# Performance work log

Measured on AMD Instinct MI355X. Metric: run time of the kernel, lower is better.

The kernel has to match this reference:

```python
import jax, jax.numpy as jnp
import numpy as np

EMBED_DIM = 1024
N_HEADS = 16
HEAD_SIZE = EMBED_DIM // N_HEADS
SEQ_LEN = 2048
BATCH = 4


def setup_inputs() -> dict:
    key = jax.random.key(0)
    ks = jax.random.split(key, 9)
    s = 0.02
    d = EMBED_DIM
    return {
        "x": jax.random.normal(ks[0], (BATCH, SEQ_LEN, d), dtype=jnp.float32),
        "wq": jax.random.normal(ks[1], (d, d), dtype=jnp.float32) * s,
        "bq": jnp.zeros((d,), dtype=jnp.float32),
        "wk": jax.random.normal(ks[2], (d, d), dtype=jnp.float32) * s,
        "bk": jnp.zeros((d,), dtype=jnp.float32),
        "wv": jax.random.normal(ks[3], (d, d), dtype=jnp.float32) * s,
        "bv": jnp.zeros((d,), dtype=jnp.float32),
        "wo": jax.random.normal(ks[4], (d, d), dtype=jnp.float32) * s,
        "bo": jnp.zeros((d,), dtype=jnp.float32),
    }


def reference(x, wq, bq, wk, bk, wv, bv, wo, bo):
    b, t, c = x.shape
    h, hs = N_HEADS, HEAD_SIZE
    scale = hs ** -0.5
    # projections (torch Linear: x @ W^T + b); here weights stored as [in, out]
    q = (x @ wq + bq).reshape(b, t, h, hs).transpose(0, 2, 1, 3)  # [b,h,t,hs]
    k = (x @ wk + bk).reshape(b, t, h, hs).transpose(0, 2, 1, 3)
    v = (x @ wv + bv).reshape(b, t, h, hs).transpose(0, 2, 1, 3)
    scores = jnp.einsum('bhqd,bhkd->bhqk', q, k) * scale  # [b,h,t,t]
    causal = jnp.tril(jnp.ones((t, t), dtype=bool))
    scores = jnp.where(causal, scores, -jnp.inf)
    probs = jax.nn.softmax(scores, axis=-1)
    attn = jnp.einsum('bhqk,bhkd->bhqd', probs, v)  # [b,h,t,hs]
    attn = attn.transpose(0, 2, 1, 3).reshape(b, t, c)
    return attn @ wo + bo
```

## Files before the change

kernel.cpp:

```cpp
#include <hip/hip_runtime.h>

#define EMBED 1024
#define NH 16
#define HS 64
#define SEQT 2048
#define NB 4

typedef unsigned short u16;
typedef unsigned int u32;
typedef __attribute__((ext_vector_type(8))) __bf16 bf16x8;
typedef __attribute__((ext_vector_type(4))) float f32x4;
typedef __attribute__((ext_vector_type(4))) unsigned short u16x4;

__device__ __forceinline__ u16 f2bf(float f) {
  __bf16 h = (__bf16)f;
  return __builtin_bit_cast(u16, h);
}

__device__ __forceinline__ void gload_lds16(const void* g, void* l) {
  __builtin_amdgcn_global_load_lds((const __attribute__((address_space(1))) void*)g,
                                   (__attribute__((address_space(3))) void*)l, 16, 0, 0);
}

#define MFMA16(a, b, c) __builtin_amdgcn_mfma_f32_16x16x32_bf16(a, b, c, 0, 0, 0)

__global__ void cvt_x(const float* __restrict__ in, u16* __restrict__ out) {
  int i = (blockIdx.x * 256 + threadIdx.x) * 4;
  float4 v = *(const float4*)(in + i);
  u16x4 o;
  o[0] = f2bf(v.x); o[1] = f2bf(v.y); o[2] = f2bf(v.z); o[3] = f2bf(v.w);
  *(u16x4*)(out + i) = o;
}

__global__ void wtrans(const float* __restrict__ w0, const float* __restrict__ w1,
                       const float* __restrict__ w2, const float* __restrict__ w3,
                       u16* __restrict__ t0, u16* __restrict__ t1,
                       u16* __restrict__ t2, u16* __restrict__ t3) {
  __shared__ float tile[32][33];
  const float* w; u16* t;
  switch (blockIdx.z) {
    case 0: w = w0; t = t0; break;
    case 1: w = w1; t = t1; break;
    case 2: w = w2; t = t2; break;
    default: w = w3; t = t3; break;
  }
  int n0 = blockIdx.x * 32, k0 = blockIdx.y * 32;
  int tx = threadIdx.x, ty = threadIdx.y;
#pragma unroll
  for (int r = 0; r < 4; ++r)
    tile[ty + r * 8][tx] = w[(size_t)(k0 + ty + r * 8) * EMBED + n0 + tx];
  __syncthreads();
#pragma unroll
  for (int r = 0; r < 4; ++r)
    t[(size_t)(n0 + ty + r * 8) * EMBED + k0 + tx] = f2bf(tile[tx][ty + r * 8]);
}

__global__ __launch_bounds__(256, 2) void gemm_qkv(
    const u16* __restrict__ A, const u16* __restrict__ Bt,
    const float* __restrict__ bq, const float* __restrict__ bk, const float* __restrict__ bv,
    u16* __restrict__ qo, u16* __restrict__ ko, u16* __restrict__ vto) {
  __shared__ __align__(16) u16 As[2][8192];
  __shared__ __align__(16) u16 Bs[2][8192];
  int m0 = blockIdx.y * 128, n0 = blockIdx.x * 128;
  int z = n0 >> 10;
  const float* bias = (z == 0) ? bq : ((z == 1) ? bk : bv);
  const float sc = (z == 0) ? 0.18033688011112042f : 1.0f;
  int tid = threadIdx.x, lane = tid & 63, wid = tid >> 6;
  int wr = wid >> 1, wc = wid & 1;
  int lr = lane & 15, lg = lane >> 4;
  const int srow_in = lane >> 3;
  const int scol_sw = ((lane & 7) ^ (lane >> 3)) * 8;
  f32x4 zero = {0.f, 0.f, 0.f, 0.f};
  f32x4 acc[4][4];
#pragma unroll
  for (int m = 0; m < 4; ++m)
#pragma unroll
    for (int n = 0; n < 4; ++n) acc[m][n] = zero;

  auto STAGE = [&](int k0, int b) {
#pragma unroll
    for (int j = 0; j < 4; ++j) {
      int rb = (j * 4 + wid) * 8;
      gload_lds16(A + (size_t)(m0 + rb + srow_in) * EMBED + k0 + scol_sw, &As[b][rb * 64]);
      gload_lds16(Bt + (size_t)(n0 + rb + srow_in) * EMBED + k0 + scol_sw, &Bs[b][rb * 64]);
    }
  };

  STAGE(0, 0);
  __syncthreads();
  int cur = 0;
  for (int k0 = 0; k0 < EMBED; k0 += 64) {
    if (k0 + 64 < EMBED) STAGE(k0 + 64, cur ^ 1);
    bf16x8 af[4][2], bfr[4][2];
#pragma unroll
    for (int m = 0; m < 4; ++m)
#pragma unroll
      for (int kk = 0; kk < 2; ++kk)
        af[m][kk] = *(const bf16x8*)(&As[cur][(wr * 64 + m * 16 + lr) * 64 +
                                              (((kk * 4 + lg) ^ (lr & 7)) * 8)]);
#pragma unroll
    for (int n = 0; n < 4; ++n)
#pragma unroll
      for (int kk = 0; kk < 2; ++kk)
        bfr[n][kk] = *(const bf16x8*)(&Bs[cur][(wc * 64 + n * 16 + lr) * 64 +
                                               (((kk * 4 + lg) ^ (lr & 7)) * 8)]);
    __builtin_amdgcn_s_setprio(1);
#pragma unroll
    for (int m = 0; m < 4; ++m)
#pragma unroll
      for (int n = 0; n < 4; ++n) {
        acc[m][n] = MFMA16(af[m][0], bfr[n][0], acc[m][n]);
        acc[m][n] = MFMA16(af[m][1], bfr[n][1], acc[m][n]);
      }
    __builtin_amdgcn_s_setprio(0);
    __syncthreads();
    cur ^= 1;
  }

#pragma unroll
  for (int n = 0; n < 4; ++n) {
    int col = n0 + wc * 64 + n * 16 + lr;
    int lcol = col & 1023;
    float bv_ = bias[lcol];
    int h = lcol >> 6, d = lcol & 63;
#pragma unroll
    for (int m = 0; m < 4; ++m) {
      int r0 = m0 + wr * 64 + m * 16 + lg * 4;
      int b_ = r0 >> 11, t_ = r0 & 2047;
      if (z < 2) {
        u16* dst = (z == 0) ? qo : ko;
#pragma unroll
        for (int i = 0; i < 4; ++i)
          dst[(((size_t)(b_ * NH + h)) * SEQT + t_ + i) * HS + d] = f2bf((acc[m][n][i] + bv_) * sc);
      } else {
        u16x4 v;
#pragma unroll
        for (int i = 0; i < 4; ++i) v[i] = f2bf(acc[m][n][i] + bv_);
        *(u16x4*)(vto + (((size_t)(b_ * NH + h)) * HS + d) * SEQT + t_) = v;
      }
    }
  }
}

__global__ __launch_bounds__(256, 3) void flash(
    const u16* __restrict__ q, const u16* __restrict__ k,
    const u16* __restrict__ vt, u16* __restrict__ attnb) {
  __shared__ __align__(16) u16 Ks[2][4096];
  __shared__ __align__(16) u16 Vs[2][4096];
  __shared__ __align__(16) u16 Pl[4][2048];
  const int tid = threadIdx.x, lane = tid & 63, wid = tid >> 6;
  const int lr = lane & 15, lg = lane >> 4;
  const int g = blockIdx.x >> 6, pair = blockIdx.x & 63;
  const int qtile = 15 - g;
  const u16* Qh = q + (size_t)pair * SEQT * HS;
  const u16* Kh = k + (size_t)pair * SEQT * HS;
  const u16* Vh = vt + (size_t)pair * HS * SEQT;

  const int sr0 = wid * 16 + (lane >> 3);
  const int sc0 = (lane & 7) ^ (sr0 & 7);
  const int sr1 = sr0 + 8;
  const int sc1 = (lane & 7) ^ (sr1 & 7);
  const int koff0 = sr0 * 64 + sc0 * 8;
  const int koff1 = sr1 * 64 + sc1 * 8;
  const size_t voff0 = (size_t)sr0 * SEQT + sc0 * 8;
  const size_t voff1 = (size_t)sr1 * SEQT + sc1 * 8;

  auto STAGE = [&](int t, int b) {
    const u16* Kb = Kh + (size_t)t * 4096;
    const u16* Vb = Vh + (size_t)t * 64;
    gload_lds16(Kb + koff0, &Ks[b][wid * 1024]);
    gload_lds16(Kb + koff1, &Ks[b][wid * 1024 + 512]);
    gload_lds16(Vb + voff0, &Vs[b][wid * 1024]);
    gload_lds16(Vb + voff1, &Vs[b][wid * 1024 + 512]);
  };

  const int b_ = pair >> 4, h = pair & 15;
  const int qw = qtile * 128 + wid * 32;

  bf16x8 qf[2][2];
#pragma unroll
  for (int nq = 0; nq < 2; ++nq)
#pragma unroll
    for (int ks = 0; ks < 2; ++ks)
      qf[nq][ks] = *(const bf16x8*)(Qh + (size_t)(qw + nq * 16 + lr) * HS + ks * 32 + lg * 8);

  f32x4 o[2][4];
  const f32x4 zero = {0.f, 0.f, 0.f, 0.f};
#pragma unroll
  for (int mr = 0; mr < 2; ++mr)
#pragma unroll
    for (int nd = 0; nd < 4; ++nd) o[mr][nd] = zero;
  float mrow[2] = {-1e30f, -1e30f}, lrow[2] = {0.f, 0.f};

  const int nt = (qtile + 1) * 2;
  int cur = 0;
  STAGE(0, 0);
  __syncthreads();

  for (int t = 0; t < nt; ++t) {
    if (t + 1 < nt) STAGE(t + 1, cur ^ 1);
    const int k0 = t * 64;

    bf16x8 kf[4][2];
#pragma unroll
    for (int mf = 0; mf < 4; ++mf) {
      const int row = mf * 16 + lr;
#pragma unroll
      for (int ks = 0; ks < 2; ++ks)
        kf[mf][ks] = *(const bf16x8*)(&Ks[cur][row * 64 + ((ks * 4 + lg) ^ (lr & 7)) * 8]);
    }
    f32x4 s[2][4];
    __builtin_amdgcn_s_setprio(1);
#pragma unroll
    for (int nq = 0; nq < 2; ++nq)
#pragma unroll
      for (int mf = 0; mf < 4; ++mf) {
        f32x4 a = zero;
        a = MFMA16(kf[mf][0], qf[nq][0], a);
        a = MFMA16(kf[mf][1], qf[nq][1], a);
        s[nq][mf] = a;
      }
    __builtin_amdgcn_s_setprio(0);
    bf16x8 vf[4][2];
#pragma unroll
    for (int nd = 0; nd < 4; ++nd) {
      const int row = nd * 16 + lr;
#pragma unroll
      for (int ks = 0; ks < 2; ++ks)
        vf[nd][ks] = *(const bf16x8*)(&Vs[cur][row * 64 + ((ks * 4 + lg) ^ (lr & 7)) * 8]);
    }

#pragma unroll
    for (int nq = 0; nq < 2; ++nq) {
      const int qmin = qw + nq * 16;
      if (k0 + 63 > qmin) {
        const int ql = qmin + lr;
#pragma unroll
        for (int mf = 0; mf < 4; ++mf) {
          const int kvb = k0 + mf * 16 + lg * 4;
#pragma unroll
          for (int r = 0; r < 4; ++r)
            if (kvb + r > ql) s[nq][mf][r] = -3.0e38f;
        }
      }
      float t0 = fmaxf(fmaxf(s[nq][0][0], s[nq][0][1]), fmaxf(s[nq][0][2], s[nq][0][3]));
      float t1 = fmaxf(fmaxf(s[nq][1][0], s[nq][1][1]), fmaxf(s[nq][1][2], s[nq][1][3]));
      float t2 = fmaxf(fmaxf(s[nq][2][0], s[nq][2][1]), fmaxf(s[nq][2][2], s[nq][2][3]));
      float t3 = fmaxf(fmaxf(s[nq][3][0], s[nq][3][1]), fmaxf(s[nq][3][2], s[nq][3][3]));
      float mx = fmaxf(fmaxf(t0, t1), fmaxf(t2, t3));
      mx = fmaxf(mx, __shfl_xor(mx, 16, 64));
      mx = fmaxf(mx, __shfl_xor(mx, 32, 64));
      if (__any(mx > mrow[nq] + 8.0f)) {
        const float mn = fmaxf(mrow[nq], mx);
        const float al = exp2f(mrow[nq] - mn);
        mrow[nq] = mn;
        lrow[nq] *= al;
        float ao[4];
#pragma unroll
        for (int r = 0; r < 4; ++r) ao[r] = __shfl(al, lg * 4 + r, 64);
#pragma unroll
        for (int nd = 0; nd < 4; ++nd)
#pragma unroll
          for (int r = 0; r < 4; ++r) o[nq][nd][r] *= ao[r];
      }
      const float mn = mrow[nq];
      float rs = 0.f;
#pragma unroll
      for (int mf = 0; mf < 4; ++mf) {
        u16x4 pk;
#pragma unroll
        for (int r = 0; r < 4; ++r) {
          const float pv = exp2f(s[nq][mf][r] - mn);
          rs += pv;
          pk[r] = f2bf(pv);
        }
        *(u16x4*)(&Pl[wid][(nq * 16 + lr) * 64 +
                           (((2 * mf + (lg >> 1)) ^ (lr & 7)) * 8 + (lg & 1) * 4)]) = pk;
      }
      rs += __shfl_xor(rs, 16, 64);
      rs += __shfl_xor(rs, 32, 64);
      lrow[nq] += rs;
    }

    bf16x8 pa[2][2];
#pragma unroll
    for (int mr = 0; mr < 2; ++mr)
#pragma unroll
      for (int ks = 0; ks < 2; ++ks)
        pa[mr][ks] = *(const bf16x8*)(&Pl[wid][(mr * 16 + lr) * 64 + ((ks * 4 + lg) ^ (lr & 7)) * 8]);
    __builtin_amdgcn_s_setprio(1);
#pragma unroll
    for (int mr = 0; mr < 2; ++mr)
#pragma unroll
      for (int nd = 0; nd < 4; ++nd) {
        o[mr][nd] = MFMA16(pa[mr][0], vf[nd][0], o[mr][nd]);
        o[mr][nd] = MFMA16(pa[mr][1], vf[nd][1], o[mr][nd]);
      }
    __builtin_amdgcn_s_setprio(0);

    __syncthreads();
    cur ^= 1;
  }

#pragma unroll
  for (int mr = 0; mr < 2; ++mr) {
    const float lv = 1.0f / lrow[mr];
    float li[4];
#pragma unroll
    for (int r = 0; r < 4; ++r) li[r] = __shfl(lv, lg * 4 + r, 64);
#pragma unroll
    for (int nd = 0; nd < 4; ++nd) {
      const int d = nd * 16 + lr;
#pragma unroll
      for (int r = 0; r < 4; ++r) {
        const int t_ = qw + mr * 16 + lg * 4 + r;
        attnb[((size_t)(b_ * SEQT + t_)) * EMBED + h * 64 + d] = f2bf(o[mr][nd][r] * li[r]);
      }
    }
  }
}

__global__ __launch_bounds__(256, 2) void gemm_out(
    const u16* __restrict__ A, const u16* __restrict__ wot,
    const float* __restrict__ bo, float* __restrict__ out) {
  __shared__ __align__(16) u16 As[2][8192];
  __shared__ __align__(16) u16 Bs[2][8192];
  int m0 = blockIdx.y * 128, n0 = blockIdx.x * 128;
  int tid = threadIdx.x, lane = tid & 63, wid = tid >> 6;
  int wr = wid >> 1, wc = wid & 1;
  int lr = lane & 15, lg = lane >> 4;
  const int srow_in = lane >> 3;
  const int scol_sw = ((lane & 7) ^ (lane >> 3)) * 8;
  f32x4 zero = {0.f, 0.f, 0.f, 0.f};
  f32x4 acc[4][4];
#pragma unroll
  for (int m = 0; m < 4; ++m)
#pragma unroll
    for (int n = 0; n < 4; ++n) acc[m][n] = zero;

  auto STAGE = [&](int k0, int b) {
#pragma unroll
    for (int j = 0; j < 4; ++j) {
      int rb = (j * 4 + wid) * 8;
      gload_lds16(A + (size_t)(m0 + rb + srow_in) * EMBED + k0 + scol_sw, &As[b][rb * 64]);
      gload_lds16(wot + (size_t)(n0 + rb + srow_in) * EMBED + k0 + scol_sw, &Bs[b][rb * 64]);
    }
  };

  STAGE(0, 0);
  __syncthreads();
  int cur = 0;
  for (int k0 = 0; k0 < EMBED; k0 += 64) {
    if (k0 + 64 < EMBED) STAGE(k0 + 64, cur ^ 1);
    bf16x8 af[4][2], bfr[4][2];
#pragma unroll
    for (int m = 0; m < 4; ++m)
#pragma unroll
      for (int kk = 0; kk < 2; ++kk)
        af[m][kk] = *(const bf16x8*)(&As[cur][(wr * 64 + m * 16 + lr) * 64 +
                                              (((kk * 4 + lg) ^ (lr & 7)) * 8)]);
#pragma unroll
    for (int n = 0; n < 4; ++n)
#pragma unroll
      for (int kk = 0; kk < 2; ++kk)
        bfr[n][kk] = *(const bf16x8*)(&Bs[cur][(wc * 64 + n * 16 + lr) * 64 +
                                               (((kk * 4 + lg) ^ (lr & 7)) * 8)]);
    __builtin_amdgcn_s_setprio(1);
#pragma unroll
    for (int m = 0; m < 4; ++m)
#pragma unroll
      for (int n = 0; n < 4; ++n) {
        acc[m][n] = MFMA16(af[m][0], bfr[n][0], acc[m][n]);
        acc[m][n] = MFMA16(af[m][1], bfr[n][1], acc[m][n]);
      }
    __builtin_amdgcn_s_setprio(0);
    __syncthreads();
    cur ^= 1;
  }

#pragma unroll
  for (int n = 0; n < 4; ++n) {
    int col = n0 + wc * 64 + n * 16 + lr;
    float bv_ = bo[col];
#pragma unroll
    for (int m = 0; m < 4; ++m) {
      int r0 = m0 + wr * 64 + m * 16 + lg * 4;
#pragma unroll
      for (int i = 0; i < 4; ++i)
        out[(size_t)(r0 + i) * EMBED + col] = acc[m][n][i] + bv_;
    }
  }
}

extern "C" void kernel_launch(void* const* d_in, const int* in_sizes, int n_in,
                              void* d_out, int out_size, void* d_ws, size_t ws_size,
                              hipStream_t stream) {
  const float* x  = (const float*)d_in[0];
  const float* wq = (const float*)d_in[1];
  const float* bq = (const float*)d_in[2];
  const float* wk = (const float*)d_in[3];
  const float* bk = (const float*)d_in[4];
  const float* wv = (const float*)d_in[5];
  const float* bv = (const float*)d_in[6];
  const float* wo = (const float*)d_in[7];
  const float* bo = (const float*)d_in[8];
  float* out = (float*)d_out;

  char* ws = (char*)d_ws;
  const size_t XB = 16777216;
  const size_t WB = 2097152;
  const size_t QB = 16777216;
  u16* xb     = (u16*)(ws);
  u16* wqkvbt = (u16*)(ws + XB);
  u16* wobt   = (u16*)(ws + XB + 3 * WB);
  u16* qb     = (u16*)(ws + XB + 4 * WB);
  u16* kb     = (u16*)(ws + XB + 4 * WB + QB);
  u16* vtb    = (u16*)(ws + XB + 4 * WB + 2 * QB);
  u16* attnb  = (u16*)(ws + XB + 4 * WB + 3 * QB);

  hipLaunchKernelGGL(cvt_x, dim3(8192), dim3(256), 0, stream, x, xb);
  hipLaunchKernelGGL(wtrans, dim3(32, 32, 4), dim3(32, 8), 0, stream,
                     wq, wk, wv, wo,
                     wqkvbt, wqkvbt + 1048576, wqkvbt + 2097152, wobt);
  hipLaunchKernelGGL(gemm_qkv, dim3(24, 64), dim3(256), 0, stream,
                     xb, wqkvbt, bq, bk, bv, qb, kb, vtb);
  hipLaunchKernelGGL(flash, dim3(1024), dim3(256), 0, stream, qb, kb, vtb, attnb);
  hipLaunchKernelGGL(gemm_out, dim3(8, 64), dim3(256), 0, stream, attnb, wobt, bo, out);
}
```

Baseline: 262.9 us.

## Restructure projection GEMMs with larger tiles, interleaved staging, and XCD-aware block swizzle

Both projection GEMMs now use a shared templated core with 512-thread blocks and larger tiles (256x256 for QKV, 128x256 for output). Each K step is split into four MFMA phases, and global-to-LDS prefetch of the next tile is spread across those phases with explicit vmcnt waits and raw barriers in place of a single syncthreads. The 1D grid is swizzled so consecutive blocks land on the same chiplet group to improve L2 reuse. The aim is to raise arithmetic intensity and overlap loads with MFMA. The cost is higher register pressure (acc[8][4] per thread) and fewer blocks, which may leave CUs idle: 384 and 256 blocks respectively.

```diff
diff --git a/kernel.cpp b/kernel.cpp
--- a/kernel.cpp
+++ b/kernel.cpp
@@ -23,6 +23,7 @@
 }
 
 #define MFMA16(a, b, c) __builtin_amdgcn_mfma_f32_16x16x32_bf16(a, b, c, 0, 0, 0)
+#define LDS_FENCE() asm volatile("" ::: "memory")
 
 __global__ void cvt_x(const float* __restrict__ in, u16* __restrict__ out) {
   int i = (blockIdx.x * 256 + threadIdx.x) * 4;
@@ -55,77 +56,165 @@
     t[(size_t)(n0 + ty + r * 8) * EMBED + k0 + tx] = f2bf(tile[tx][ty + r * 8]);
 }
 
-__global__ __launch_bounds__(256, 2) void gemm_qkv(
+template <int BM, int MREP>
+__device__ __forceinline__ void gemm_core(
+    const u16* __restrict__ A, const u16* __restrict__ Bt, int m0, int n0,
+    u16 (&As)[2][BM * 64], u16 (&Bs)[2][256 * 64],
+    f32x4 (&acc)[MREP][4], int lane, int wid) {
+  const int tid = wid * 64 + lane;
+  const int lr = lane & 15, lg = lane >> 4;
+  const int arow = tid >> 3;
+  const int csw = ((tid & 7) ^ (arow & 7)) * 8;
+  const int ldst = arow * 64 + (tid & 7) * 8;
+  const int wrb = (wid >> 2) * (BM / 2);
+  const int wcb = (wid & 3) * 64;
+  const u16* Aa = A + (size_t)m0 * EMBED;
+  const u16* Bb = Bt + (size_t)n0 * EMBED;
+
+  auto stage = [&](const u16* src, u16* dst, int j, int k0) {
+    gload_lds16(src + (size_t)(arow + 64 * j) * EMBED + k0 + csw, dst + j * 4096 + ldst);
+  };
+  auto rd = [&](const u16* buf, int row, int kk) -> bf16x8 {
+    return *(const bf16x8*)(buf + row * 64 + (((kk * 4 + lg) ^ (lr & 7)) * 8));
+  };
+
+#pragma unroll
+  for (int j = 0; j < BM / 64; ++j) stage(Aa, As[0], j, 0);
+#pragma unroll
+  for (int j = 0; j < 4; ++j) stage(Bb, Bs[0], j, 0);
+
+  for (int t = 0; t < 16; ++t) {
+    const int kn = (t + 1) * 64;
+    u16* Ac = (t & 1) ? As[1] : As[0];
+    u16* Bc = (t & 1) ? Bs[1] : Bs[0];
+    u16* An = (t & 1) ? As[0] : As[1];
+    u16* Bn = (t & 1) ? Bs[0] : Bs[1];
+    const bool pf = (t < 15);
+
+    bf16x8 af[MREP / 2][2], bf0[2][2], bf1[2][2];
+
+    if (pf) {
+      stage(Aa, An, 0, kn);
+      if constexpr (BM == 256) {
+        stage(Aa, An, 1, kn);
+        asm volatile("s_waitcnt vmcnt(2)" ::: "memory");
+      } else {
+        asm volatile("s_waitcnt vmcnt(1)" ::: "memory");
+      }
+    } else {
+      asm volatile("s_waitcnt vmcnt(0)" ::: "memory");
+    }
+    __builtin_amdgcn_sched_barrier(0);
+    __builtin_amdgcn_s_barrier();
+    LDS_FENCE();
+#pragma unroll
+    for (int mi = 0; mi < MREP / 2; ++mi)
+#pragma unroll
+      for (int kk = 0; kk < 2; ++kk) af[mi][kk] = rd(Ac, wrb + mi * 16 + lr, kk);
+#pragma unroll
+    for (int ni = 0; ni < 2; ++ni)
+#pragma unroll
+      for (int kk = 0; kk < 2; ++kk) bf0[ni][kk] = rd(Bc, wcb + ni * 16 + lr, kk);
+    __builtin_amdgcn_s_setprio(1);
+#pragma unroll
+    for (int mi = 0; mi < MREP / 2; ++mi)
+#pragma unroll
+      for (int ni = 0; ni < 2; ++ni) {
+        acc[mi][ni] = MFMA16(af[mi][0], bf0[ni][0], acc[mi][ni]);
+        acc[mi][ni] = MFMA16(af[mi][1], bf0[ni][1], acc[mi][ni]);
+      }
+    __builtin_amdgcn_s_setprio(0);
+    __builtin_amdgcn_s_barrier();
+    LDS_FENCE();
+
+    if (pf) {
+      if constexpr (BM == 256) { stage(Aa, An, 2, kn); stage(Aa, An, 3, kn); }
+      else stage(Aa, An, 1, kn);
+    }
+#pragma unroll
+    for (int ni = 0; ni < 2; ++ni)
+#pragma unroll
+      for (int kk = 0; kk < 2; ++kk) bf1[ni][kk] = rd(Bc, wcb + (2 + ni) * 16 + lr, kk);
+    __builtin_amdgcn_s_setprio(1);
+#pragma unroll
+    for (int mi = 0; mi < MREP / 2; ++mi)
+#pragma unroll
+      for (int ni = 0; ni < 2; ++ni) {
+        acc[mi][2 + ni] = MFMA16(af[mi][0], bf1[ni][0], acc[mi][2 + ni]);
+        acc[mi][2 + ni] = MFMA16(af[mi][1], bf1[ni][1], acc[mi][2 + ni]);
+      }
+    __builtin_amdgcn_s_setprio(0);
+    __builtin_amdgcn_s_barrier();
+    LDS_FENCE();
+
+    if (pf) { stage(Bb, Bn, 0, kn); stage(Bb, Bn, 1, kn); }
+#pragma unroll
+    for (int mi = 0; mi < MREP / 2; ++mi)
+#pragma unroll
+      for (int kk = 0; kk < 2; ++kk)
+        af[mi][kk] = rd(Ac, wrb + (MREP / 2 + mi) * 16 + lr, kk);
+    __builtin_amdgcn_s_setprio(1);
+#pragma unroll
+    for (int mi = 0; mi < MREP / 2; ++mi)
+#pragma unroll
+      for (int ni = 0; ni < 2; ++ni) {
+        acc[MREP / 2 + mi][2 + ni] = MFMA16(af[mi][0], bf1[ni][0], acc[MREP / 2 + mi][2 + ni]);
+        acc[MREP / 2 + mi][2 + ni] = MFMA16(af[mi][1], bf1[ni][1], acc[MREP / 2 + mi][2 + ni]);
+      }
+    __builtin_amdgcn_s_setprio(0);
+    __builtin_amdgcn_s_barrier();
+    LDS_FENCE();
+
+    if (pf) { stage(Bb, Bn, 2, kn); stage(Bb, Bn, 3, kn); }
+    __builtin_amdgcn_s_setprio(1);
+#pragma unroll
+    for (int mi = 0; mi < MREP / 2; ++mi)
+#pragma unroll
+      for (int ni = 0; ni < 2; ++ni) {
+        acc[MREP / 2 + mi][ni] = MFMA16(af[mi][0], bf0[ni][0], acc[MREP / 2 + mi][ni]);
+        acc[MREP / 2 + mi][ni] = MFMA16(af[mi][1], bf0[ni][1], acc[MREP / 2 + mi][ni]);
+      }
+    __builtin_amdgcn_s_setprio(0);
+    __builtin_amdgcn_s_barrier();
+    LDS_FENCE();
+  }
+}
+
+__global__ __launch_bounds__(512, 2) void gemm_qkv(
     const u16* __restrict__ A, const u16* __restrict__ Bt,
     const float* __restrict__ bq, const float* __restrict__ bk, const float* __restrict__ bv,
     u16* __restrict__ qo, u16* __restrict__ ko, u16* __restrict__ vto) {
-  __shared__ __align__(16) u16 As[2][8192];
-  __shared__ __align__(16) u16 Bs[2][8192];
-  int m0 = blockIdx.y * 128, n0 = blockIdx.x * 128;
-  int z = n0 >> 10;
+  __shared__ __align__(16) u16 As[2][256 * 64];
+  __shared__ __align__(16) u16 Bs[2][256 * 64];
+  const int bid = blockIdx.x;
+  const int swz = (bid & 7) * 48 + (bid >> 3);
+  const int bm = swz / 12, bn = swz % 12;
+  const int m0 = bm * 256, n0 = bn * 256;
+  const int lane = threadIdx.x & 63, wid = threadIdx.x >> 6;
+  const int lr = lane & 15, lg = lane >> 4;
+  const int z = n0 >> 10;
   const float* bias = (z == 0) ? bq : ((z == 1) ? bk : bv);
   const float sc = (z == 0) ? 0.18033688011112042f : 1.0f;
-  int tid = threadIdx.x, lane = tid & 63, wid = tid >> 6;
-  int wr = wid >> 1, wc = wid & 1;
-  int lr = lane & 15, lg = lane >> 4;
-  const int srow_in = lane >> 3;
-  const int scol_sw = ((lane & 7) ^ (lane >> 3)) * 8;
-  f32x4 zero = {0.f, 0.f, 0.f, 0.f};
-  f32x4 acc[4][4];
-#pragma unroll
-  for (int m = 0; m < 4; ++m)
+
+  f32x4 acc[8][4];
+  const f32x4 zero = {0.f, 0.f, 0.f, 0.f};
+#pragma unroll
+  for (int m = 0; m < 8; ++m)
 #pragma unroll
     for (int n = 0; n < 4; ++n) acc[m][n] = zero;
 
-  auto STAGE = [&](int k0, int b) {
-#pragma unroll
-    for (int j = 0; j < 4; ++j) {
-      int rb = (j * 4 + wid) * 8;
-      gload_lds16(A + (size_t)(m0 + rb + srow_in) * EMBED + k0 + scol_sw, &As[b][rb * 64]);
-      gload_lds16(Bt + (size_t)(n0 + rb + srow_in) * EMBED + k0 + scol_sw, &Bs[b][rb * 64]);
-    }
-  };
-
-  STAGE(0, 0);
-  __syncthreads();
-  int cur = 0;
-  for (int k0 = 0; k0 < EMBED; k0 += 64) {
-    if (k0 + 64 < EMBED) STAGE(k0 + 64, cur ^ 1);
-    bf16x8 af[4][2], bfr[4][2];
-#pragma unroll
-    for (int m = 0; m < 4; ++m)
-#pragma unroll
-      for (int kk = 0; kk < 2; ++kk)
-        af[m][kk] = *(const bf16x8*)(&As[cur][(wr * 64 + m * 16 + lr) * 64 +
-                                              (((kk * 4 + lg) ^ (lr & 7)) * 8)]);
-#pragma unroll
-    for (int n = 0; n < 4; ++n)
-#pragma unroll
-      for (int kk = 0; kk < 2; ++kk)
-        bfr[n][kk] = *(const bf16x8*)(&Bs[cur][(wc * 64 + n * 16 + lr) * 64 +
-                                               (((kk * 4 + lg) ^ (lr & 7)) * 8)]);
-    __builtin_amdgcn_s_setprio(1);
-#pragma unroll
-    for (int m = 0; m < 4; ++m)
-#pragma unroll
-      for (int n = 0; n < 4; ++n) {
-        acc[m][n] = MFMA16(af[m][0], bfr[n][0], acc[m][n]);
-        acc[m][n] = MFMA16(af[m][1], bfr[n][1], acc[m][n]);
-      }
-    __builtin_amdgcn_s_setprio(0);
-    __syncthreads();
-    cur ^= 1;
-  }
-
+  gemm_core<256, 8>(A, Bt, m0, n0, As, Bs, acc, lane, wid);
+
+  const int wrb = (wid >> 2) * 128, wcb = (wid & 3) * 64;
 #pragma unroll
   for (int n = 0; n < 4; ++n) {
-    int col = n0 + wc * 64 + n * 16 + lr;
+    int col = n0 + wcb + n * 16 + lr;
     int lcol = col & 1023;
     float bv_ = bias[lcol];
     int h = lcol >> 6, d = lcol & 63;
 #pragma unroll
-    for (int m = 0; m < 4; ++m) {
-      int r0 = m0 + wr * 64 + m * 16 + lg * 4;
+    for (int m = 0; m < 8; ++m) {
+      int r0 = m0 + wrb + m * 16 + lg * 4;
       int b_ = r0 >> 11, t_ = r0 & 2047;
       if (z < 2) {
         u16* dst = (z == 0) ? qo : ko;
@@ -138,6 +227,42 @@
         for (int i = 0; i < 4; ++i) v[i] = f2bf(acc[m][n][i] + bv_);
         *(u16x4*)(vto + (((size_t)(b_ * NH + h)) * HS + d) * SEQT + t_) = v;
       }
+    }
+  }
+}
+
+__global__ __launch_bounds__(512, 2) void gemm_out(
+    const u16* __restrict__ A, const u16* __restrict__ wot,
+    const float* __restrict__ bo, float* __restrict__ out) {
+  __shared__ __align__(16) u16 As[2][128 * 64];
+  __shared__ __align__(16) u16 Bs[2][256 * 64];
+  const int bid = blockIdx.x;
+  const int swz = (bid & 7) * 32 + (bid >> 3);
+  const int bm = swz >> 2, bn = swz & 3;
+  const int m0 = bm * 128, n0 = bn * 256;
+  const int lane = threadIdx.x & 63, wid = threadIdx.x >> 6;
+  const int lr = lane & 15, lg = lane >> 4;
+
+  f32x4 acc[4][4];
+  const f32x4 zero = {0.f, 0.f, 0.f, 0.f};
+#pragma unroll
+  for (int m = 0; m < 4; ++m)
+#pragma unroll
+    for (int n = 0; n < 4; ++n) acc[m][n] = zero;
+
+  gemm_core<128, 4>(A, wot, m0, n0, As, Bs, acc, lane, wid);
+
+  const int wrb = (wid >> 2) * 64, wcb = (wid & 3) * 64;
+#pragma unroll
+  for (int n = 0; n < 4; ++n) {
+    int col = n0 + wcb + n * 16 + lr;
+    float bv_ = bo[col];
+#pragma unroll
+    for (int m = 0; m < 4; ++m) {
+      int r0 = m0 + wrb + m * 16 + lg * 4;
+#pragma unroll
+      for (int i = 0; i < 4; ++i)
+        out[(size_t)(r0 + i) * EMBED + col] = acc[m][n][i] + bv_;
     }
   }
 }
@@ -320,78 +445,6 @@
   }
 }
 
-__global__ __launch_bounds__(256, 2) void gemm_out(
-    const u16* __restrict__ A, const u16* __restrict__ wot,
-    const float* __restrict__ bo, float* __restrict__ out) {
-  __shared__ __align__(16) u16 As[2][8192];
-  __shared__ __align__(16) u16 Bs[2][8192];
-  int m0 = blockIdx.y * 128, n0 = blockIdx.x * 128;
-  int tid = threadIdx.x, lane = tid & 63, wid = tid >> 6;
-  int wr = wid >> 1, wc = wid & 1;
-  int lr = lane & 15, lg = lane >> 4;
-  const int srow_in = lane >> 3;
-  const int scol_sw = ((lane & 7) ^ (lane >> 3)) * 8;
-  f32x4 zero = {0.f, 0.f, 0.f, 0.f};
-  f32x4 acc[4][4];
-#pragma unroll
-  for (int m = 0; m < 4; ++m)
-#pragma unroll
-    for (int n = 0; n < 4; ++n) acc[m][n] = zero;
-
-  auto STAGE = [&](int k0, int b) {
-#pragma unroll
-    for (int j = 0; j < 4; ++j) {
-      int rb = (j * 4 + wid) * 8;
-      gload_lds16(A + (size_t)(m0 + rb + srow_in) * EMBED + k0 + scol_sw, &As[b][rb * 64]);
-      gload_lds16(wot + (size_t)(n0 + rb + srow_in) * EMBED + k0 + scol_sw, &Bs[b][rb * 64]);
-    }
-  };
-
-  STAGE(0, 0);
-  __syncthreads();
-  int cur = 0;
-  for (int k0 = 0; k0 < EMBED; k0 += 64) {
-    if (k0 + 64 < EMBED) STAGE(k0 + 64, cur ^ 1);
-    bf16x8 af[4][2], bfr[4][2];
-#pragma unroll
-    for (int m = 0; m < 4; ++m)
-#pragma unroll
-      for (int kk = 0; kk < 2; ++kk)
-        af[m][kk] = *(const bf16x8*)(&As[cur][(wr * 64 + m * 16 + lr) * 64 +
-                                              (((kk * 4 + lg) ^ (lr & 7)) * 8)]);
-#pragma unroll
-    for (int n = 0; n < 4; ++n)
-#pragma unroll
-      for (int kk = 0; kk < 2; ++kk)
-        bfr[n][kk] = *(const bf16x8*)(&Bs[cur][(wc * 64 + n * 16 + lr) * 64 +
-                                               (((kk * 4 + lg) ^ (lr & 7)) * 8)]);
-    __builtin_amdgcn_s_setprio(1);
-#pragma unroll
-    for (int m = 0; m < 4; ++m)
-#pragma unroll
-      for (int n = 0; n < 4; ++n) {
-        acc[m][n] = MFMA16(af[m][0], bfr[n][0], acc[m][n]);
-        acc[m][n] = MFMA16(af[m][1], bfr[n][1], acc[m][n]);
-      }
-    __builtin_amdgcn_s_setprio(0);
-    __syncthreads();
-    cur ^= 1;
-  }
-
-#pragma unroll
-  for (int n = 0; n < 4; ++n) {
-    int col = n0 + wc * 64 + n * 16 + lr;
-    float bv_ = bo[col];
-#pragma unroll
-    for (int m = 0; m < 4; ++m) {
-      int r0 = m0 + wr * 64 + m * 16 + lg * 4;
-#pragma unroll
-      for (int i = 0; i < 4; ++i)
-        out[(size_t)(r0 + i) * EMBED + col] = acc[m][n][i] + bv_;
-    }
-  }
-}
-
 extern "C" void kernel_launch(void* const* d_in, const int* in_sizes, int n_in,
                               void* d_out, int out_size, void* d_ws, size_t ws_size,
                               hipStream_t stream) {
@@ -422,8 +475,8 @@
   hipLaunchKernelGGL(wtrans, dim3(32, 32, 4), dim3(32, 8), 0, stream,
                      wq, wk, wv, wo,
                      wqkvbt, wqkvbt + 1048576, wqkvbt + 2097152, wobt);
-  hipLaunchKernelGGL(gemm_qkv, dim3(24, 64), dim3(256), 0, stream,
+  hipLaunchKernelGGL(gemm_qkv, dim3(384), dim3(512), 0, stream,
                      xb, wqkvbt, bq, bk, bv, qb, kb, vtb);
   hipLaunchKernelGGL(flash, dim3(1024), dim3(256), 0, stream, qb, kb, vtb, attnb);
-  hipLaunchKernelGGL(gemm_out, dim3(8, 64), dim3(256), 0, stream, attnb, wobt, bo, out);
-}
+  hipLaunchKernelGGL(gemm_out, dim3(256), dim3(512), 0, stream, attnb, wobt, bo, out);
+}
```

New measurement: 280.0 us. 1.07x slower.
